# Kernel optimization log

Hardware: AMD Instinct MI355X
Metric: run time of the kernel (lower is better)

Reference implementation:

```python
import jax, jax.numpy as jnp
import numpy as np

N_DOWN, N_ABOVE, D_IN, D_OUT, FAN_IN = 50000, 100000, 256, 256, 5


def setup_inputs() -> dict:
    key = jax.random.key(0)
    ks = jax.random.split(key, 8)
    h = jax.random.normal(ks[0], (N_DOWN, D_IN), dtype=jnp.float32)
    h_above = jax.random.normal(ks[1], (N_ABOVE, D_IN), dtype=jnp.float32)  # only shape[0] used
    # idx: unique positions of the down nodes within the up-node index space
    idx = jax.random.permutation(ks[2], N_ABOVE)[:N_DOWN]
    # fixed fan-in 5: destination ids i are each node repeated 5 times (DGL bucketing order)
    i = jnp.repeat(jnp.arange(N_ABOVE), FAN_IN)
    j = jax.random.randint(ks[3], (N_ABOVE * FAN_IN,), 0, N_ABOVE)
    s1 = 1.0 / np.sqrt(D_IN * FAN_IN)
    s2 = 1.0 / np.sqrt(D_OUT)
    W1 = jax.random.uniform(ks[4], (D_IN * FAN_IN, D_OUT), jnp.float32, -s1, s1)
    b1 = jax.random.uniform(ks[5], (D_OUT,), jnp.float32, -s1, s1)
    W2 = jax.random.uniform(ks[6], (D_OUT, D_OUT), jnp.float32, -s2, s2)
    b2 = jax.random.uniform(ks[7], (D_OUT,), jnp.float32, -s2, s2)
    return {"h": h, "h_above": h_above, "idx": idx, "i": i, "j": j,
            "W1": W1, "b1": b1, "W2": W2, "b2": b2}


def reference(h, h_above, idx, i, j, W1, b1, W2, b2):
    n_above = h_above.shape[0]
    d = h.shape[1]
    # scatter down-node features into the up-node index space (new_h[idx] = h)
    new_h = jnp.zeros((n_above, d), dtype=h.dtype).at[idx].set(h)
    # gather the 5 source-node messages per destination; i = repeat(arange, 5),
    # so j grouped in blocks of 5 corresponds to each destination's mailbox.
    gathered = new_h[j].reshape(n_above, 5 * d)  # [n_above, 5*d]
    hid = jax.nn.relu(gathered @ W1 + b1)
    return hid @ W2 + b2
```

## Files before the change

### kernel.cpp

```cpp
#include <hip/hip_runtime.h>

#define N_DOWN  50000
#define N_ABOVE 100000
#define DIM     256
#define FAN     5
#define K1      1280
#define MPAD    100096

typedef __bf16 bf16x8 __attribute__((ext_vector_type(8)));
typedef float  f32x4  __attribute__((ext_vector_type(4)));

__device__ __forceinline__ unsigned short f2bf(float f) {
  unsigned u = __builtin_bit_cast(unsigned, f);
  u += 0x7FFFu + ((u >> 16) & 1u);
  return (unsigned short)(u >> 16);
}

__device__ __forceinline__ void gload16(const unsigned short* g, unsigned short* l) {
  __builtin_amdgcn_global_load_lds(
      (const __attribute__((address_space(1))) void*)g,
      (__attribute__((address_space(3))) void*)l, 16, 0, 0);
}

__global__ void k_prep_inv(int* __restrict__ inv, unsigned short* __restrict__ hbf) {
  int t = blockIdx.x * 256 + threadIdx.x;
  if (t < N_ABOVE) inv[t] = N_DOWN;
  if (t < DIM)     hbf[(size_t)N_DOWN * DIM + t] = 0;
}

__device__ __forceinline__ void transpose_tile(const float* __restrict__ in,
                                               unsigned short* __restrict__ out,
                                               int K, int N, int k0, int n0,
                                               float (*tile)[65]) {
  int c = threadIdx.x & 63, rb = threadIdx.x >> 6;
#pragma unroll
  for (int rr = 0; rr < 16; ++rr) {
    int row = rb + rr * 4;
    tile[row][c] = in[(size_t)(k0 + row) * N + n0 + c];
  }
  __syncthreads();
#pragma unroll
  for (int rr = 0; rr < 16; ++rr) {
    int nr = rb + rr * 4;
    out[(size_t)(n0 + nr) * K + k0 + c] = f2bf(tile[c][nr]);
  }
}

__global__ void k_prep_all(const float* __restrict__ h, const int* __restrict__ idx,
                           const float* __restrict__ W1, const float* __restrict__ W2,
                           int* __restrict__ inv, unsigned short* __restrict__ hbf,
                           unsigned short* __restrict__ w1t, unsigned short* __restrict__ w2t) {
  __shared__ float tile[64][65];
  const int b = blockIdx.x;
  if (b < 12500) {
    int t = b * 256 + threadIdx.x;
    float4 v = ((const float4*)h)[t];
    ushort4 o;
    o.x = f2bf(v.x); o.y = f2bf(v.y); o.z = f2bf(v.z); o.w = f2bf(v.w);
    ((ushort4*)hbf)[t] = o;
  } else if (b < 12696) {
    int t = (b - 12500) * 256 + threadIdx.x;
    if (t < N_DOWN) inv[idx[t]] = t;
  } else if (b < 12776) {
    int bb = b - 12696;
    transpose_tile(W1, w1t, K1, DIM, (bb % 20) * 64, (bb / 20) * 64, tile);
  } else {
    int bb = b - 12776;
    transpose_tile(W2, w2t, DIM, DIM, (bb % 4) * 64, (bb / 4) * 64, tile);
  }
}

__global__ __launch_bounds__(256, 2) void k_gemm1(
    const unsigned short* __restrict__ hbf,
    const unsigned short* __restrict__ w1t,
    const float* __restrict__ b1,
    const int* __restrict__ inv,
    const int* __restrict__ jarr,
    unsigned short* __restrict__ hid)
{
  __shared__ __align__(16) unsigned short Alds[128 * 64];
  __shared__ __align__(16) unsigned short Blds[128 * 64];
  __shared__ int srcrow[128 * FAN];

  const int tid = threadIdx.x;
  const int w = tid >> 6, l = tid & 63;
  const int m0 = blockIdx.x * 128, n0 = blockIdx.y * 128;
  const int wm = w >> 1, wn = w & 1;
  const int srow = l >> 3, slot = l & 7;

  for (int e = tid; e < 128 * FAN; e += 256) {
    int row = e / FAN, rr = e - row * FAN;
    int gm = m0 + row;
    int s = N_DOWN;
    if (gm < N_ABOVE) s = inv[jarr[(size_t)gm * FAN + rr]];
    srcrow[e] = s;
  }

  f32x4 acc[4][4] = {};

  for (int t = 0; t < 20; ++t) {
    const int r = t >> 2;
    __syncthreads();
#pragma unroll
    for (int i = 0; i < 4; ++i) {
      int row = w * 32 + i * 8 + srow;
      int src = srcrow[row * FAN + r];
      int c = slot ^ (row & 7);
      gload16(hbf + ((size_t)src << 8) + ((t & 3) << 6) + (c << 3),
              Alds + (w * 32 + i * 8) * 64);
    }
#pragma unroll
    for (int i = 0; i < 4; ++i) {
      int row = w * 32 + i * 8 + srow;
      int c = slot ^ (row & 7);
      gload16(w1t + (size_t)(n0 + row) * K1 + (t << 6) + (c << 3),
              Blds + (w * 32 + i * 8) * 64);
    }
    __syncthreads();

#pragma unroll
    for (int kk = 0; kk < 2; ++kk) {
      bf16x8 af[4], bfr[4];
#pragma unroll
      for (int m = 0; m < 4; ++m) {
        int row = wm * 64 + m * 16 + (l & 15);
        int c = (kk * 4 + (l >> 4)) ^ (row & 7);
        af[m] = *(const bf16x8*)(Alds + row * 64 + c * 8);
      }
#pragma unroll
      for (int n = 0; n < 4; ++n) {
        int row = wn * 64 + n * 16 + (l & 15);
        int c = (kk * 4 + (l >> 4)) ^ (row & 7);
        bfr[n] = *(const bf16x8*)(Blds + row * 64 + c * 8);
      }
#pragma unroll
      for (int m = 0; m < 4; ++m)
#pragma unroll
        for (int n = 0; n < 4; ++n)
          acc[m][n] = __builtin_amdgcn_mfma_f32_16x16x32_bf16(af[m], bfr[n], acc[m][n], 0, 0, 0);
    }
  }

  float bias0 = b1[n0 + wn * 64 + 0 * 16 + (l & 15)];
  float bias1 = b1[n0 + wn * 64 + 1 * 16 + (l & 15)];
  float bias2 = b1[n0 + wn * 64 + 2 * 16 + (l & 15)];
  float bias3 = b1[n0 + wn * 64 + 3 * 16 + (l & 15)];
#pragma unroll
  for (int m = 0; m < 4; ++m) {
#pragma unroll
    for (int q = 0; q < 4; ++q) {
      int gm = m0 + wm * 64 + m * 16 + (l >> 4) * 4 + q;
#pragma unroll
      for (int n = 0; n < 4; ++n) {
        float bias = n == 0 ? bias0 : n == 1 ? bias1 : n == 2 ? bias2 : bias3;
        int gn = n0 + wn * 64 + n * 16 + (l & 15);
        float v = acc[m][n][q] + bias;
        v = v > 0.f ? v : 0.f;
        hid[(size_t)gm * DIM + gn] = f2bf(v);
      }
    }
  }
}

__global__ __launch_bounds__(512, 2) void k_gemm2(
    const unsigned short* __restrict__ hid,
    const unsigned short* __restrict__ w2t,
    const float* __restrict__ b2,
    float* __restrict__ out)
{
  __shared__ __align__(16) unsigned short Alds[128 * 64];
  __shared__ __align__(16) unsigned short Blds[256 * 64];

  const int tid = threadIdx.x;
  const int w = tid >> 6, l = tid & 63;
  const int m0 = blockIdx.x * 128;
  const int wm = w >> 2, wn = w & 3;
  const int srow = l >> 3, slot = l & 7;

  f32x4 acc[4][4] = {};

  for (int t = 0; t < 4; ++t) {
    __syncthreads();
#pragma unroll
    for (int i = 0; i < 2; ++i) {
      int row = w * 16 + i * 8 + srow;
      int c = slot ^ (row & 7);
      gload16(hid + (size_t)(m0 + row) * DIM + (t << 6) + (c << 3),
              Alds + (w * 16 + i * 8) * 64);
    }
#pragma unroll
    for (int i = 0; i < 4; ++i) {
      int row = w * 32 + i * 8 + srow;
      int c = slot ^ (row & 7);
      gload16(w2t + (size_t)row * DIM + (t << 6) + (c << 3),
              Blds + (w * 32 + i * 8) * 64);
    }
    __syncthreads();

#pragma unroll
    for (int kk = 0; kk < 2; ++kk) {
      bf16x8 af[4], bfr[4];
#pragma unroll
      for (int m = 0; m < 4; ++m) {
        int row = wm * 64 + m * 16 + (l & 15);
        int c = (kk * 4 + (l >> 4)) ^ (row & 7);
        af[m] = *(const bf16x8*)(Alds + row * 64 + c * 8);
      }
#pragma unroll
      for (int n = 0; n < 4; ++n) {
        int row = wn * 64 + n * 16 + (l & 15);
        int c = (kk * 4 + (l >> 4)) ^ (row & 7);
        bfr[n] = *(const bf16x8*)(Blds + row * 64 + c * 8);
      }
#pragma unroll
      for (int m = 0; m < 4; ++m)
#pragma unroll
        for (int n = 0; n < 4; ++n)
          acc[m][n] = __builtin_amdgcn_mfma_f32_16x16x32_bf16(af[m], bfr[n], acc[m][n], 0, 0, 0);
    }
  }

  float bias0 = b2[wn * 64 + 0 * 16 + (l & 15)];
  float bias1 = b2[wn * 64 + 1 * 16 + (l & 15)];
  float bias2 = b2[wn * 64 + 2 * 16 + (l & 15)];
  float bias3 = b2[wn * 64 + 3 * 16 + (l & 15)];
#pragma unroll
  for (int m = 0; m < 4; ++m) {
#pragma unroll
    for (int q = 0; q < 4; ++q) {
      int gm = m0 + wm * 64 + m * 16 + (l >> 4) * 4 + q;
      if (gm < N_ABOVE) {
#pragma unroll
        for (int n = 0; n < 4; ++n) {
          float bias = n == 0 ? bias0 : n == 1 ? bias1 : n == 2 ? bias2 : bias3;
          int gn = wn * 64 + n * 16 + (l & 15);
          out[(size_t)gm * DIM + gn] = acc[m][n][q] + bias;
        }
      }
    }
  }
}

extern "C" void kernel_launch(void* const* d_in, const int* in_sizes, int n_in,
                              void* d_out, int out_size, void* d_ws, size_t ws_size,
                              hipStream_t stream) {
  const float* h    = (const float*)d_in[0];
  const int*   idx  = (const int*)d_in[2];
  const int*   jarr = (const int*)d_in[4];
  const float* W1   = (const float*)d_in[5];
  const float* b1   = (const float*)d_in[6];
  const float* W2   = (const float*)d_in[7];
  const float* b2   = (const float*)d_in[8];
  float* out = (float*)d_out;

  char* ws = (char*)d_ws;
  size_t off = 0;
  auto alloc = [&](size_t bytes) -> void* {
    void* p = ws + off;
    off += bytes;
    off = (off + 511) & ~(size_t)511;
    return p;
  };
  int*            inv = (int*)alloc((size_t)N_ABOVE * 4);
  unsigned short* hbf = (unsigned short*)alloc((size_t)(N_DOWN + 1) * DIM * 2);
  unsigned short* w1t = (unsigned short*)alloc((size_t)DIM * K1 * 2);
  unsigned short* w2t = (unsigned short*)alloc((size_t)DIM * DIM * 2);
  unsigned short* hid = (unsigned short*)alloc((size_t)MPAD * DIM * 2);
  if (ws_size < off) return;

  k_prep_inv<<<dim3(391), dim3(256), 0, stream>>>(inv, hbf);
  k_prep_all<<<dim3(12792), dim3(256), 0, stream>>>(h, idx, W1, W2, inv, hbf, w1t, w2t);
  k_gemm1<<<dim3(MPAD / 128, 2), dim3(256), 0, stream>>>(hbf, w1t, b1, inv, jarr, hid);
  k_gemm2<<<dim3(MPAD / 128), dim3(512), 0, stream>>>(hid, w2t, b2, out);
}
```

Baseline: 124.4 us.

## Replace inv-init kernel with memsets, shrink srcrow, load GEMM2 operands directly

The separate init kernel is replaced by two hipMemsetAsync calls, which fill inv with -1; gemm1 now maps negative entries to the zero row. The gemm1 srcrow table is stored as 16-bit shorts to cut shared memory. gemm2 drops its LDS staging and syncthreads and reads MFMA fragments straight from global memory through the cache. This removes a launch and the barrier overhead, at the cost of uncoalesced 16-byte global reads and redundant re-reads of the W2 operand across waves.

```diff
diff --git a/kernel.cpp b/kernel.cpp
--- a/kernel.cpp
+++ b/kernel.cpp
@@ -20,12 +20,6 @@
   __builtin_amdgcn_global_load_lds(
       (const __attribute__((address_space(1))) void*)g,
       (__attribute__((address_space(3))) void*)l, 16, 0, 0);
-}
-
-__global__ void k_prep_inv(int* __restrict__ inv, unsigned short* __restrict__ hbf) {
-  int t = blockIdx.x * 256 + threadIdx.x;
-  if (t < N_ABOVE) inv[t] = N_DOWN;
-  if (t < DIM)     hbf[(size_t)N_DOWN * DIM + t] = 0;
 }
 
 __device__ __forceinline__ void transpose_tile(const float* __restrict__ in,
@@ -80,7 +74,7 @@
 {
   __shared__ __align__(16) unsigned short Alds[128 * 64];
   __shared__ __align__(16) unsigned short Blds[128 * 64];
-  __shared__ int srcrow[128 * FAN];
+  __shared__ unsigned short srcrow[128 * FAN];
 
   const int tid = threadIdx.x;
   const int w = tid >> 6, l = tid & 63;
@@ -92,8 +86,11 @@
     int row = e / FAN, rr = e - row * FAN;
     int gm = m0 + row;
     int s = N_DOWN;
-    if (gm < N_ABOVE) s = inv[jarr[(size_t)gm * FAN + rr]];
-    srcrow[e] = s;
+    if (gm < N_ABOVE) {
+      s = inv[jarr[(size_t)gm * FAN + rr]];
+      if (s < 0) s = N_DOWN;
+    }
+    srcrow[e] = (unsigned short)s;
   }
 
   f32x4 acc[4][4] = {};
@@ -162,62 +159,35 @@
   }
 }
 
-__global__ __launch_bounds__(512, 2) void k_gemm2(
+__global__ __launch_bounds__(512) void k_gemm2(
     const unsigned short* __restrict__ hid,
     const unsigned short* __restrict__ w2t,
     const float* __restrict__ b2,
     float* __restrict__ out)
 {
-  __shared__ __align__(16) unsigned short Alds[128 * 64];
-  __shared__ __align__(16) unsigned short Blds[256 * 64];
-
   const int tid = threadIdx.x;
   const int w = tid >> 6, l = tid & 63;
   const int m0 = blockIdx.x * 128;
   const int wm = w >> 2, wn = w & 3;
-  const int srow = l >> 3, slot = l & 7;
+  const int rowA = m0 + wm * 64 + (l & 15);
+  const int rowB = wn * 64 + (l & 15);
+  const int kb   = (l >> 4) * 8;
 
   f32x4 acc[4][4] = {};
-
-  for (int t = 0; t < 4; ++t) {
-    __syncthreads();
-#pragma unroll
-    for (int i = 0; i < 2; ++i) {
-      int row = w * 16 + i * 8 + srow;
-      int c = slot ^ (row & 7);
-      gload16(hid + (size_t)(m0 + row) * DIM + (t << 6) + (c << 3),
-              Alds + (w * 16 + i * 8) * 64);
-    }
-#pragma unroll
-    for (int i = 0; i < 4; ++i) {
-      int row = w * 32 + i * 8 + srow;
-      int c = slot ^ (row & 7);
-      gload16(w2t + (size_t)row * DIM + (t << 6) + (c << 3),
-              Blds + (w * 32 + i * 8) * 64);
-    }
-    __syncthreads();
-
-#pragma unroll
-    for (int kk = 0; kk < 2; ++kk) {
-      bf16x8 af[4], bfr[4];
-#pragma unroll
-      for (int m = 0; m < 4; ++m) {
-        int row = wm * 64 + m * 16 + (l & 15);
-        int c = (kk * 4 + (l >> 4)) ^ (row & 7);
-        af[m] = *(const bf16x8*)(Alds + row * 64 + c * 8);
-      }
-#pragma unroll
-      for (int n = 0; n < 4; ++n) {
-        int row = wn * 64 + n * 16 + (l & 15);
-        int c = (kk * 4 + (l >> 4)) ^ (row & 7);
-        bfr[n] = *(const bf16x8*)(Blds + row * 64 + c * 8);
-      }
-#pragma unroll
-      for (int m = 0; m < 4; ++m)
-#pragma unroll
-        for (int n = 0; n < 4; ++n)
-          acc[m][n] = __builtin_amdgcn_mfma_f32_16x16x32_bf16(af[m], bfr[n], acc[m][n], 0, 0, 0);
-    }
+#pragma unroll 2
+  for (int t = 0; t < 8; ++t) {
+    bf16x8 af[4], bfr[4];
+#pragma unroll
+    for (int mf = 0; mf < 4; ++mf)
+      af[mf] = *(const bf16x8*)(hid + (size_t)(rowA + mf * 16) * DIM + t * 32 + kb);
+#pragma unroll
+    for (int nf = 0; nf < 4; ++nf)
+      bfr[nf] = *(const bf16x8*)(w2t + (size_t)(rowB + nf * 16) * DIM + t * 32 + kb);
+#pragma unroll
+    for (int mf = 0; mf < 4; ++mf)
+#pragma unroll
+      for (int nf = 0; nf < 4; ++nf)
+        acc[mf][nf] = __builtin_amdgcn_mfma_f32_16x16x32_bf16(af[mf], bfr[nf], acc[mf][nf], 0, 0, 0);
   }
 
   float bias0 = b2[wn * 64 + 0 * 16 + (l & 15)];
@@ -268,7 +238,8 @@
   unsigned short* hid = (unsigned short*)alloc((size_t)MPAD * DIM * 2);
   if (ws_size < off) return;
 
-  k_prep_inv<<<dim3(391), dim3(256), 0, stream>>>(inv, hbf);
+  hipMemsetAsync(inv, 0xFF, (size_t)N_ABOVE * 4, stream);
+  hipMemsetAsync(hbf + (size_t)N_DOWN * DIM, 0, DIM * 2, stream);
   k_prep_all<<<dim3(12792), dim3(256), 0, stream>>>(h, idx, W1, W2, inv, hbf, w1t, w2t);
   k_gemm1<<<dim3(MPAD / 128, 2), dim3(256), 0, stream>>>(hbf, w1t, b1, inv, jarr, hid);
   k_gemm2<<<dim3(MPAD / 128), dim3(512), 0, stream>>>(hid, w2t, b2, out);
```

Result: slower. 167.9 us (+34.9%).
